# Kernel optimization log

Hardware: AMD Instinct MI355X
Metric: run time of the kernel (lower is better)

## Reference

```python
import jax, jax.numpy as jnp
import numpy as np

B, T, C, H = 2, 2048, 1024, 16
D = C // H  # head_dim = 64


def setup_inputs() -> dict:
    key = jax.random.key(0)
    k1, k2, k3 = jax.random.split(key, 3)
    x = jax.random.normal(k1, (B, T, C), dtype=jnp.float32)
    Wqkv = jax.random.normal(k2, (C, 3 * C), dtype=jnp.float32) * (1.0 / np.sqrt(C))
    Wo = jax.random.normal(k3, (C, C), dtype=jnp.float32) * (1.0 / np.sqrt(C))
    bo = jnp.zeros((C,), dtype=jnp.float32)
    return {"x": x, "Wqkv": Wqkv, "Wo": Wo, "bo": bo}


def reference(x, Wqkv, Wo, bo):
    Bc, Tc, Cc = x.shape
    qkv = x @ Wqkv                                  # [B,T,3C]
    q, k, v = jnp.split(qkv, 3, axis=-1)
    # [B,T,C] -> [B,H,T,D]
    q = q.reshape(Bc, Tc, H, D).transpose(0, 2, 1, 3)
    k = k.reshape(Bc, Tc, H, D).transpose(0, 2, 1, 3)
    v = v.reshape(Bc, Tc, H, D).transpose(0, 2, 1, 3)
    scale = 1.0 / np.sqrt(D)
    att = jnp.einsum('bhqd,bhkd->bhqk', q, k) * scale   # [B,H,T,T]
    causal = jnp.tril(jnp.ones((Tc, Tc), dtype=bool))
    att = jnp.where(causal[None, None], att, -jnp.inf)
    att = jax.nn.softmax(att, axis=-1)
    # dropout treated as identity (eval mode)
    y = jnp.einsum('bhqk,bhkd->bhqd', att, v)           # [B,H,T,D]
    y = y.transpose(0, 2, 1, 3).reshape(Bc, Tc, Cc)     # [B,T,C]
    return y @ Wo + bo
```

## Files before the change

kernel.cpp:

```cpp
#include <hip/hip_runtime.h>
#include <hip/hip_bf16.h>
#include <math.h>


typedef __attribute__((ext_vector_type(8))) short bf16x8;
typedef __attribute__((ext_vector_type(4))) float f32x4;

__device__ __forceinline__ float b2f(unsigned short u) {
    union { unsigned int i; float f; } x; x.i = ((unsigned int)u) << 16; return x.f;
}
__device__ __forceinline__ unsigned short f2b(float f) {
    __hip_bfloat16 h = __float2bfloat16(f);
    return *reinterpret_cast<unsigned short*>(&h);
}
__device__ __forceinline__ unsigned short f2b_rz(float f) {
    union { float f; unsigned int i; } u; u.f = f; return (unsigned short)(u.i >> 16);
}
__device__ __forceinline__ float fexp2(float x) {
#if __has_builtin(__builtin_amdgcn_exp2f)
    return __builtin_amdgcn_exp2f(x);
#else
    return exp2f(x);
#endif
}
__device__ __forceinline__ void gload_lds16(const void* g, void* l) {
    __builtin_amdgcn_global_load_lds(
        (__attribute__((address_space(1))) void*)g,
        (__attribute__((address_space(3))) void*)l, 16, 0, 0);
}

__device__ __forceinline__ void transpose_job64(
        const void* __restrict__ in, unsigned short* __restrict__ out,
        int Cc, int use_bf, int nscale, float scale,
        int c0, int r0, int tid, unsigned short (*t)[65]) {
    const unsigned short* inb = (const unsigned short*)in;
    const float* inf = (const float*)in;
    const int x = tid & 63, y = tid >> 6;
    #pragma unroll
    for (int i = 0; i < 64; i += 4) {
        size_t idx = (size_t)(r0 + y + i) * Cc + c0 + x;
        float v = use_bf ? b2f(inb[idx]) : inf[idx];
        if (c0 + x < nscale) v *= scale;
        t[y + i][x] = f2b(v);
    }
    __syncthreads();
    #pragma unroll
    for (int i = 0; i < 64; i += 4)
        out[(size_t)(c0 + y + i) * 1024 + r0 + x] = t[x][y + i];
}

__global__ __launch_bounds__(256) void prep_kernel(
        const void* __restrict__ xin, const void* __restrict__ Wqkv,
        const void* __restrict__ Wo, const void* __restrict__ bias,
        unsigned short* __restrict__ xb, unsigned short* __restrict__ WqkvT,
        unsigned short* __restrict__ WoT, unsigned short* __restrict__ bob,
        int* __restrict__ flag, float qscale) {
    __shared__ __align__(16) unsigned short t[64][65];
    __shared__ int det;
    const int tid = threadIdx.x, blk = blockIdx.x;

    if (tid < 64) {
        const unsigned short* xu = (const unsigned short*)xin;
        int cnt = 0;
        for (int i = tid; i < 1024; i += 64) {
            unsigned short u = xu[2 * i];
            int e = (u >> 7) & 0xFF;
            if (!((e == 0) || (e >= 96 && e <= 159))) cnt++;
        }
        #pragma unroll
        for (int m = 1; m < 64; m <<= 1) cnt += __shfl_xor(cnt, m);
        if (tid == 0) det = (cnt > 200) ? 0 : 1;
    }
    __syncthreads();
    const int use_bf = det;

    if (blk < 1024) {
        int base = blk * 4096;
        #pragma unroll
        for (int i = 0; i < 4; i++) {
            int i4 = base + (tid + 256 * i) * 4;
            if (use_bf) {
                *(ushort4*)(xb + i4) = *(const ushort4*)((const unsigned short*)xin + i4);
            } else {
                float4 f = *(const float4*)((const float*)xin + i4);
                ushort4 o;
                o.x = f2b(f.x); o.y = f2b(f.y); o.z = f2b(f.z); o.w = f2b(f.w);
                *(ushort4*)(xb + i4) = o;
            }
        }
    } else if (blk < 1792) {
        int tt = blk - 1024;
        int c0 = (tt % 48) * 64, r0 = (tt / 48) * 64;
        transpose_job64(Wqkv, WqkvT, 3072, use_bf, 1024, qscale, c0, r0, tid, t);
    } else if (blk < 2048) {
        int tt = blk - 1792;
        int c0 = (tt & 15) * 64, r0 = (tt >> 4) * 64;
        transpose_job64(Wo, WoT, 1024, use_bf, 0, 1.0f, c0, r0, tid, t);
    } else {
        int i4 = tid * 4;
        if (use_bf) {
            *(ushort4*)(bob + i4) = *(const ushort4*)((const unsigned short*)bias + i4);
        } else {
            float4 f = *(const float4*)((const float*)bias + i4);
            ushort4 o;
            o.x = f2b(f.x); o.y = f2b(f.y); o.z = f2b(f.z); o.w = f2b(f.w);
            *(ushort4*)(bob + i4) = o;
        }
        if (tid == 0) *flag = use_bf;
    }
}

__global__ __launch_bounds__(256) void gemm_qkv(
        const unsigned short* __restrict__ A, const unsigned short* __restrict__ Bt,
        unsigned short* __restrict__ qb, unsigned short* __restrict__ kb,
        unsigned short* __restrict__ vt) {
    __shared__ __align__(16) unsigned short lA[128 * 64];
    __shared__ __align__(16) unsigned short lB[64 * 64];
    const int tid  = threadIdx.x;
    const int wave = tid >> 6, lane = tid & 63;
    const int g = lane >> 4, c = lane & 15;
    const int m0 = blockIdx.y * 128, n0 = blockIdx.x * 64;
    const int wm = wave * 32;
    const int srow = lane >> 3;
    const int sc8  = ((lane & 7) ^ ((lane >> 3) & 7)) * 8;

    f32x4 acc[2][4] = {};

    for (int k0 = 0; k0 < 1024; k0 += 64) {
        #pragma unroll
        for (int i = 0; i < 4; i++) {
            int seg = wave * 4 + i;
            int row = seg * 8 + srow;
            gload_lds16(A + (size_t)(m0 + row) * 1024 + k0 + sc8, lA + seg * 512);
        }
        #pragma unroll
        for (int i = 0; i < 2; i++) {
            int seg = wave * 2 + i;
            int row = seg * 8 + srow;
            gload_lds16(Bt + (size_t)(n0 + row) * 1024 + k0 + sc8, lB + seg * 512);
        }
        __syncthreads();

        #pragma unroll
        for (int dk = 0; dk < 2; dk++) {
            const int off = ((4 * dk + g) ^ (c & 7)) << 3;
            bf16x8 af[2], bfv[4];
            #pragma unroll
            for (int i = 0; i < 2; i++)
                af[i]  = *(const bf16x8*)(lA + (wm + 16 * i + c) * 64 + off);
            #pragma unroll
            for (int i = 0; i < 4; i++)
                bfv[i] = *(const bf16x8*)(lB + (16 * i + c) * 64 + off);
            #pragma unroll
            for (int mi = 0; mi < 2; mi++)
                #pragma unroll
                for (int ni = 0; ni < 4; ni++)
                    acc[mi][ni] = __builtin_amdgcn_mfma_f32_16x16x32_bf16(
                        af[mi], bfv[ni], acc[mi][ni], 0, 0, 0);
        }
        __syncthreads();
    }

    if (n0 < 2048) {
        unsigned short* dst = (n0 < 1024) ? qb : kb;
        int cb = n0 & 1023;
        #pragma unroll
        for (int mi = 0; mi < 2; mi++)
            #pragma unroll
            for (int ni = 0; ni < 4; ni++)
                #pragma unroll
                for (int r = 0; r < 4; r++) {
                    int row = m0 + wm + 16 * mi + 4 * g + r;
                    dst[(size_t)row * 1024 + cb + 16 * ni + c] = f2b(acc[mi][ni][r]);
                }
    } else {
        const int bb = m0 >> 11;
        const int kvb = (m0 & 2047) + wm;
        const int hb = (n0 - 2048) >> 6;
        #pragma unroll
        for (int mi = 0; mi < 2; mi++)
            #pragma unroll
            for (int ni = 0; ni < 4; ni++) {
                int d = 16 * ni + c;
                int bh = bb * 16 + hb;
                int kv = kvb + 16 * mi + 4 * g;
                ushort4 pk;
                pk.x = f2b(acc[mi][ni][0]); pk.y = f2b(acc[mi][ni][1]);
                pk.z = f2b(acc[mi][ni][2]); pk.w = f2b(acc[mi][ni][3]);
                *(ushort4*)(vt + ((size_t)bh * 64 + d) * 2048 + kv) = pk;
            }
    }
}

__global__ __launch_bounds__(256) void gemm_nt(
        const unsigned short* __restrict__ A, const unsigned short* __restrict__ Bt,
        void* __restrict__ C, const unsigned short* __restrict__ bias,
        const int* __restrict__ out_f32_flag, int M, int N, int K) {
    __shared__ __align__(16) unsigned short lA[128 * 64];
    __shared__ __align__(16) unsigned short lB[64 * 64];
    const int tid  = threadIdx.x;
    const int wave = tid >> 6, lane = tid & 63;
    const int g = lane >> 4, c = lane & 15;
    const int m0 = blockIdx.y * 128, n0 = blockIdx.x * 64;
    const int wm = wave * 32;
    const int srow = lane >> 3;
    const int sc8  = ((lane & 7) ^ ((lane >> 3) & 7)) * 8;

    f32x4 acc[2][4] = {};

    for (int k0 = 0; k0 < K; k0 += 64) {
        #pragma unroll
        for (int i = 0; i < 4; i++) {
            int seg = wave * 4 + i;
            int row = seg * 8 + srow;
            gload_lds16(A + (size_t)(m0 + row) * K + k0 + sc8, lA + seg * 512);
        }
        #pragma unroll
        for (int i = 0; i < 2; i++) {
            int seg = wave * 2 + i;
            int row = seg * 8 + srow;
            gload_lds16(Bt + (size_t)(n0 + row) * K + k0 + sc8, lB + seg * 512);
        }
        __syncthreads();

        #pragma unroll
        for (int dk = 0; dk < 2; dk++) {
            const int off = ((4 * dk + g) ^ (c & 7)) << 3;
            bf16x8 af[2], bfv[4];
            #pragma unroll
            for (int i = 0; i < 2; i++)
                af[i]  = *(const bf16x8*)(lA + (wm + 16 * i + c) * 64 + off);
            #pragma unroll
            for (int i = 0; i < 4; i++)
                bfv[i] = *(const bf16x8*)(lB + (16 * i + c) * 64 + off);
            #pragma unroll
            for (int mi = 0; mi < 2; mi++)
                #pragma unroll
                for (int ni = 0; ni < 4; ni++)
                    acc[mi][ni] = __builtin_amdgcn_mfma_f32_16x16x32_bf16(
                        af[mi], bfv[ni], acc[mi][ni], 0, 0, 0);
        }
        __syncthreads();
    }

    const bool f32out = out_f32_flag && (*out_f32_flag == 0);
    #pragma unroll
    for (int mi = 0; mi < 2; mi++)
        #pragma unroll
        for (int ni = 0; ni < 4; ni++)
            #pragma unroll
            for (int r = 0; r < 4; r++) {
                int row = m0 + wm + 16 * mi + 4 * g + r;
                int col = n0 + 16 * ni + c;
                float v = acc[mi][ni][r];
                if (bias) v += b2f(bias[col]);
                if (f32out) ((float*)C)[(size_t)row * N + col] = v;
                else ((unsigned short*)C)[(size_t)row * N + col] = f2b(v);
            }
}

template<bool MASKED>
__device__ __forceinline__ void tile_compute(
        const unsigned short* __restrict__ lKs, const unsigned short* __restrict__ lVts,
        unsigned short* __restrict__ P, const bf16x8* qB, f32x4* o,
        float& l_run, int wave, int lane, int g, int c) {
    const f32x4 sinit = {-12.f, -12.f, -12.f, -12.f};
    f32x4 s[4] = {sinit, sinit, sinit, sinit};
    #pragma unroll
    for (int nt = 0; nt < 4; nt++)
        #pragma unroll
        for (int dk = 0; dk < 2; dk++) {
            bf16x8 kA = *(const bf16x8*)(lKs + (16 * nt + c) * 64 + (((4 * dk + g) ^ (c & 7)) << 3));
            s[nt] = __builtin_amdgcn_mfma_f32_16x16x32_bf16(kA, qB[dk], s[nt], 0, 0, 0);
        }

    float rsum = 0.f;
    #pragma unroll
    for (int nt = 0; nt < 4; nt++) {
        unsigned long long pk = 0;
        #pragma unroll
        for (int r = 0; r < 4; r++) {
            float v = s[nt][r];
            if (MASKED) v = (16 * nt + 4 * g + r <= 16 * wave + c) ? v : -1e30f;
            float p = fexp2(v);
            rsum += p;
            pk |= ((unsigned long long)f2b_rz(p)) << (16 * r);
        }
        int kvl = 16 * nt + 4 * g;
        *(unsigned long long*)(P + c * 64 + (((kvl >> 3) ^ (c & 7)) << 3) + (kvl & 7)) = pk;
    }
    rsum += __shfl_xor(rsum, 16);
    rsum += __shfl_xor(rsum, 32);
    l_run += rsum;

    __asm__ volatile("s_waitcnt lgkmcnt(0)" ::: "memory");

    bf16x8 pf[2];
    #pragma unroll
    for (int kk = 0; kk < 2; kk++)
        pf[kk] = *(const bf16x8*)(P + c * 64 + (((4 * kk + g) ^ (c & 7)) << 3));
    #pragma unroll
    for (int ni = 0; ni < 4; ni++)
        #pragma unroll
        for (int kk = 0; kk < 2; kk++) {
            bf16x8 vf = *(const bf16x8*)(lVts + (16 * ni + c) * 64 + (((4 * kk + g) ^ (c & 7)) << 3));
            o[ni] = __builtin_amdgcn_mfma_f32_16x16x32_bf16(pf[kk], vf, o[ni], 0, 0, 0);
        }
    __asm__ volatile("" ::: "memory");
}

__global__ __launch_bounds__(256) void attn_kernel(
        const unsigned short* __restrict__ qb, const unsigned short* __restrict__ kb,
        const unsigned short* __restrict__ vt, unsigned short* __restrict__ Y) {
    __shared__ __align__(16) unsigned short lK[2][4096];
    __shared__ __align__(16) unsigned short lVt[2][4096];
    __shared__ __align__(16) unsigned short Pbuf[4][1024];

    const int tid = threadIdx.x, wave = tid >> 6, lane = tid & 63;
    const int g = lane >> 4, c = lane & 15;
    unsigned short* P = Pbuf[wave];
    const int srow = lane >> 3;
    const int sc8  = ((lane & 7) ^ ((lane >> 3) & 7)) * 8;

    const int rr = blockIdx.x >> 8, cc = blockIdx.x & 255;
    const int kslot = cc >> 3;
    const int j  = (rr & 1) ? kslot : (31 - kslot);
    const int bh = rr * 8 + (cc & 7);
    const int q0 = j * 64;
    const int b = bh >> 4, h = bh & 15;
    const int rbase = q0 + 16 * wave;

    const unsigned short* Qb  = qb + (size_t)b * 2048 * 1024 + h * 64;
    const unsigned short* Kb  = kb + (size_t)b * 2048 * 1024 + h * 64;
    const unsigned short* Vtb = vt + (size_t)bh * 64 * 2048;

    bf16x8 qB[2];
    #pragma unroll
    for (int dk = 0; dk < 2; dk++)
        qB[dk] = *(const bf16x8*)(Qb + (size_t)(rbase + c) * 1024 + 32 * dk + 8 * g);

    f32x4 o[4] = {};
    float l_run = 0.f;

    #pragma unroll 1
    for (int kv0 = 0; kv0 <= q0; kv0 += 128) {
        const bool do1 = (kv0 + 64 <= q0);
        #pragma unroll
        for (int i = 0; i < 2; i++) {
            int seg = wave * 2 + i;
            int row = seg * 8 + srow;
            gload_lds16(Kb  + (size_t)(kv0 + row) * 1024 + sc8, lK[0] + seg * 512);
            gload_lds16(Vtb + (size_t)row * 2048 + kv0 + sc8,   lVt[0] + seg * 512);
            if (do1) {
                gload_lds16(Kb  + (size_t)(kv0 + 64 + row) * 1024 + sc8, lK[1] + seg * 512);
                gload_lds16(Vtb + (size_t)row * 2048 + kv0 + 64 + sc8,   lVt[1] + seg * 512);
            }
        }
        __syncthreads();

        if (kv0 == q0)
            tile_compute<true >(lK[0], lVt[0], P, qB, o, l_run, wave, lane, g, c);
        else
            tile_compute<false>(lK[0], lVt[0], P, qB, o, l_run, wave, lane, g, c);
        if (do1) {
            if (kv0 + 64 == q0)
                tile_compute<true >(lK[1], lVt[1], P, qB, o, l_run, wave, lane, g, c);
            else
                tile_compute<false>(lK[1], lVt[1], P, qB, o, l_run, wave, lane, g, c);
        }
        __syncthreads();
    }

    float inv = 1.f / l_run;
    float il[4];
    #pragma unroll
    for (int r = 0; r < 4; r++)
        il[r] = __shfl(inv, (lane & 48) | (4 * g + r));
    #pragma unroll
    for (int ni = 0; ni < 4; ni++)
        #pragma unroll
        for (int r = 0; r < 4; r++) {
            int row = rbase + 4 * g + r;
            Y[(size_t)(b * 2048 + row) * 1024 + h * 64 + 16 * ni + c] =
                f2b(o[ni][r] * il[r]);
        }
}

extern "C" void kernel_launch(void* const* d_in, const int* in_sizes, int n_in,
                              void* d_out, int out_size, void* d_ws, size_t ws_size,
                              hipStream_t stream) {
    char* ws = (char*)d_ws;
    unsigned short* qb    = (unsigned short*)(ws);
    unsigned short* kb    = (unsigned short*)(ws + 8388608);
    unsigned short* vt    = (unsigned short*)(ws + 16777216);
    unsigned short* Y     = (unsigned short*)(ws + 25165824);
    unsigned short* WqkvT = (unsigned short*)(ws + 33554432);
    unsigned short* WoT   = (unsigned short*)(ws + 39845888);
    unsigned short* xb    = (unsigned short*)(ws + 41943040);
    unsigned short* bob   = (unsigned short*)(ws + 50331648);
    int*            flag  = (int*)(ws + 50333696);

    prep_kernel<<<2049, 256, 0, stream>>>(
        d_in[0], d_in[1], d_in[2], d_in[3], xb, WqkvT, WoT, bob, flag,
        0.125f * 1.4426950408889634f);

    gemm_qkv<<<dim3(48, 32), 256, 0, stream>>>(xb, WqkvT, qb, kb, vt);

    attn_kernel<<<1024, 256, 0, stream>>>(qb, kb, vt, Y);

    gemm_nt<<<dim3(16, 32), 256, 0, stream>>>(Y, WoT, d_out, bob, flag, 4096, 1024, 1024);
}
```

Before: 183.4 us.

## Double-buffer K/V tiles to prefetch the next tile during attention compute

Replaces the attention inner loop, which loaded two 64-row K/V tiles and then computed both, with a per-tile loop that alternates between two LDS buffers. At each step it issues the global-to-LDS loads for tile t+1 before computing tile t. The aim is to hide memory latency behind the MFMA and softmax work and to drop to one barrier per tile. In exchange, each 128-key span now takes two barriers instead of two, the loads are smaller and more numerous, and correctness relies on the barrier waiting for the async LDS loads to finish.

```diff
diff --git a/kernel.cpp b/kernel.cpp
--- a/kernel.cpp
+++ b/kernel.cpp
@@ -342,33 +342,29 @@
     f32x4 o[4] = {};
     float l_run = 0.f;
 
-    #pragma unroll 1
-    for (int kv0 = 0; kv0 <= q0; kv0 += 128) {
-        const bool do1 = (kv0 + 64 <= q0);
+    auto stage = [&](int t) {
+        unsigned short* dK = lK[t & 1];
+        unsigned short* dV = lVt[t & 1];
+        const int kv0 = t * 64;
         #pragma unroll
         for (int i = 0; i < 2; i++) {
             int seg = wave * 2 + i;
             int row = seg * 8 + srow;
-            gload_lds16(Kb  + (size_t)(kv0 + row) * 1024 + sc8, lK[0] + seg * 512);
-            gload_lds16(Vtb + (size_t)row * 2048 + kv0 + sc8,   lVt[0] + seg * 512);
-            if (do1) {
-                gload_lds16(Kb  + (size_t)(kv0 + 64 + row) * 1024 + sc8, lK[1] + seg * 512);
-                gload_lds16(Vtb + (size_t)row * 2048 + kv0 + 64 + sc8,   lVt[1] + seg * 512);
-            }
-        }
+            gload_lds16(Kb  + (size_t)(kv0 + row) * 1024 + sc8, dK + seg * 512);
+            gload_lds16(Vtb + (size_t)row * 2048 + kv0 + sc8,   dV + seg * 512);
+        }
+    };
+
+    stage(0);
+    const int jmax = j;
+    #pragma unroll 1
+    for (int t = 0; t <= jmax; t++) {
         __syncthreads();
-
-        if (kv0 == q0)
-            tile_compute<true >(lK[0], lVt[0], P, qB, o, l_run, wave, lane, g, c);
+        if (t < jmax) stage(t + 1);
+        if (t == jmax)
+            tile_compute<true >(lK[t & 1], lVt[t & 1], P, qB, o, l_run, wave, lane, g, c);
         else
-            tile_compute<false>(lK[0], lVt[0], P, qB, o, l_run, wave, lane, g, c);
-        if (do1) {
-            if (kv0 + 64 == q0)
-                tile_compute<true >(lK[1], lVt[1], P, qB, o, l_run, wave, lane, g, c);
-            else
-                tile_compute<false>(lK[1], lVt[1], P, qB, o, l_run, wave, lane, g, c);
-        }
-        __syncthreads();
+            tile_compute<false>(lK[t & 1], lVt[t & 1], P, qB, o, l_run, wave, lane, g, c);
     }
 
     float inv = 1.f / l_run;
```

After: 185.4 us. No clear change (+1.1%).
